# Kernel optimization log

Hardware: AMD Instinct MI355X
Metric: run time of the kernel (lower is better)

## Reference

```python
import jax, jax.numpy as jnp
import numpy as np
import math

D_MODEL = 1024
NUM_HEADS = 16
D_HEAD = D_MODEL // NUM_HEADS
SEQ = 2048
BATCH = 2
THETA = 10000.0
SCALE = 1.0 / math.sqrt(D_HEAD)


def rope_cos_sin(seq_len, d_head, theta):
    # freqs_cis equivalent: angles[t, j] = t * theta**(-2j/d_head)
    inv_freq = 1.0 / (theta ** (jnp.arange(0, d_head, 2, dtype=jnp.float32) / d_head))
    t = jnp.arange(seq_len, dtype=jnp.float32)
    ang = jnp.outer(t, inv_freq)  # [S, d_head//2]
    return jnp.cos(ang), jnp.sin(ang)


def apply_rope(x, cos, sin):
    # x: [B, S, H, Dh]; treat consecutive pairs as complex numbers
    B, S, H, Dh = x.shape
    xr = x.reshape(B, S, H, Dh // 2, 2)
    x0, x1 = xr[..., 0], xr[..., 1]
    c = cos[None, :, None, :]
    s = sin[None, :, None, :]
    out = jnp.stack([x0 * c - x1 * s, x0 * s + x1 * c], axis=-1)
    return out.reshape(B, S, H, Dh)


def setup_inputs() -> dict:
    key = jax.random.key(0)
    ks = jax.random.split(key, 9)
    w_std = 0.02
    return {
        "qkv": jax.random.normal(ks[0], (BATCH, SEQ, D_MODEL), jnp.float32),
        "Wq": jax.random.normal(ks[1], (D_MODEL, D_MODEL), jnp.float32) * w_std,
        "bq": jax.random.normal(ks[2], (D_MODEL,), jnp.float32) * w_std,
        "Wk": jax.random.normal(ks[3], (D_MODEL, D_MODEL), jnp.float32) * w_std,
        "bk": jax.random.normal(ks[4], (D_MODEL,), jnp.float32) * w_std,
        "Wv": jax.random.normal(ks[5], (D_MODEL, D_MODEL), jnp.float32) * w_std,
        "bv": jax.random.normal(ks[6], (D_MODEL,), jnp.float32) * w_std,
        "Wo": jax.random.normal(ks[7], (D_MODEL, D_MODEL), jnp.float32) * w_std,
        "bo": jax.random.normal(ks[8], (D_MODEL,), jnp.float32) * w_std,
    }


def reference(qkv, Wq, bq, Wk, bk, Wv, bv, Wo, bo):
    B, S, D = qkv.shape
    cos, sin = rope_cos_sin(S, D_HEAD, THETA)
    # torch Linear: y = x @ W.T + b
    q = (qkv @ Wq.T + bq).reshape(B, S, NUM_HEADS, D_HEAD)
    k = (qkv @ Wk.T + bk).reshape(B, S, NUM_HEADS, D_HEAD)
    v = (qkv @ Wv.T + bv).reshape(B, S, NUM_HEADS, D_HEAD)
    q = apply_rope(q, cos, sin)
    k = apply_rope(k, cos, sin)
    scores = jnp.einsum("bqhd,bkhd->bhqk", q, k) * SCALE
    causal = jnp.triu(jnp.ones((S, S), dtype=bool), k=1)
    scores = jnp.where(causal[None, None], -1e30, scores)
    attn = jax.nn.softmax(scores, axis=-1)
    out = jnp.einsum("bhqk,bkhd->bqhd", attn, v).reshape(B, S, D)
    return out @ Wo.T + bo
```

## Files before the change

### kernel.cpp

```cpp
#include <hip/hip_runtime.h>
#include <hip/hip_bf16.h>
#include <stdint.h>
#include <math.h>


typedef __bf16 bf16;
typedef __attribute__((ext_vector_type(4))) __bf16 bf16x4;
typedef __attribute__((ext_vector_type(8))) __bf16 bf16x8;
typedef __attribute__((ext_vector_type(4))) float f32x4;
typedef __attribute__((ext_vector_type(16))) float f32x16;
typedef __attribute__((ext_vector_type(4))) uint32_t u32x4;

#define SEQN 2048
#define DMOD 1024
#define NHEAD 16
#define DHEAD 64
#define MTOT 4096
#define VSTR 2080
#define QSCALE_LOG2E 0.18033688011112042f

__device__ __forceinline__ void gload_lds16(const bf16* g, bf16* l) {
  __builtin_amdgcn_global_load_lds(
      (const __attribute__((address_space(1))) uint32_t*)g,
      (__attribute__((address_space(3))) uint32_t*)l,
      16, 0, 0);
}

__device__ __forceinline__ uint32_t cvtpk(float lo, float hi) {
  uint32_t r;
  asm("v_cvt_pk_bf16_f32 %0, %1, %2" : "=v"(r) : "v"(lo), "v"(hi));
  return r;
}

__global__ __launch_bounds__(256) void prep_kernel(
    const float* __restrict__ X,
    const float* __restrict__ Wq, const float* __restrict__ Wk,
    const float* __restrict__ Wv, const float* __restrict__ Wo,
    bf16* __restrict__ Xb, bf16* __restrict__ Wqb, bf16* __restrict__ Wkb,
    bf16* __restrict__ Wvb, bf16* __restrict__ Wob,
    float* __restrict__ ctab, float* __restrict__ stab)
{
  const int tid = blockIdx.x * blockDim.x + threadIdx.x;
  const int nth = gridDim.x * blockDim.x;

  const float4* X4 = (const float4*)X;
  for (int i = tid; i < MTOT * DMOD / 4; i += nth) {
    float4 v = X4[i];
    bf16x4 o = { (bf16)v.x, (bf16)v.y, (bf16)v.z, (bf16)v.w };
    *(bf16x4*)(Xb + (size_t)i * 4) = o;
  }
  const float4* q4 = (const float4*)Wq;
  const float4* k4 = (const float4*)Wk;
  const float4* v4 = (const float4*)Wv;
  const float4* o4 = (const float4*)Wo;
  for (int i = tid; i < DMOD * DMOD / 4; i += nth) {
    float4 a = q4[i];
    float4 b = k4[i];
    float4 c = v4[i];
    float4 d = o4[i];
    *(bf16x4*)(Wqb + (size_t)i * 4) = bf16x4{ (bf16)a.x, (bf16)a.y, (bf16)a.z, (bf16)a.w };
    *(bf16x4*)(Wkb + (size_t)i * 4) = bf16x4{ (bf16)b.x, (bf16)b.y, (bf16)b.z, (bf16)b.w };
    *(bf16x4*)(Wvb + (size_t)i * 4) = bf16x4{ (bf16)c.x, (bf16)c.y, (bf16)c.z, (bf16)c.w };
    *(bf16x4*)(Wob + (size_t)i * 4) = bf16x4{ (bf16)d.x, (bf16)d.y, (bf16)d.z, (bf16)d.w };
  }
  for (int i = tid; i < SEQN * 32; i += nth) {
    const int s = i >> 5, p = i & 31;
    const float invf = (float)pow(10000.0, -(double)p / 32.0);
    const float ang = (float)s * invf;
    float sv, cv;
    sincosf(ang, &sv, &cv);
    ctab[i] = cv;
    stab[i] = sv;
  }
}

__global__ __launch_bounds__(256) void gemm_qkv(
    const bf16* __restrict__ Xb,
    const bf16* __restrict__ Wqb, const bf16* __restrict__ Wkb, const bf16* __restrict__ Wvb,
    const float* __restrict__ bq, const float* __restrict__ bk, const float* __restrict__ bv,
    const float* __restrict__ ctab, const float* __restrict__ stab,
    bf16* __restrict__ Qb, bf16* __restrict__ Kb, bf16* __restrict__ Vtb)
{
  __shared__ bf16 sA[128 * 32];
  __shared__ bf16 sB[128 * 32];

  const int z = blockIdx.z;
  const bf16* Bm = (z == 0) ? Wqb : (z == 1) ? Wkb : Wvb;
  const float* bias = (z == 0) ? bq : (z == 1) ? bk : bv;

  const int t = threadIdx.x;
  const int lane = t & 63, l15 = lane & 15, g = lane >> 4;
  const int wave = t >> 6, wm = wave >> 1, wn = wave & 1;
  const int tileM = blockIdx.y * 128, tileN = blockIdx.x * 128;

  f32x4 acc[4][4] = {};

  const int srow = t >> 2, schk = t & 3;
  const bf16* gA = Xb + (size_t)(tileM + srow) * DMOD + schk * 8;
  const bf16* gB = Bm + (size_t)(tileN + srow) * DMOD + schk * 8;
  bf16* lA = sA + t * 8;
  bf16* lB = sB + t * 8;

  for (int k0 = 0; k0 < DMOD; k0 += 32) {
    __syncthreads();
    gload_lds16(gA + k0, lA);
    gload_lds16(gA + k0 + 64 * DMOD, lA + 2048);
    gload_lds16(gB + k0, lB);
    gload_lds16(gB + k0 + 64 * DMOD, lB + 2048);
    __syncthreads();
    bf16x8 af[4], bfr[4];
#pragma unroll
    for (int i = 0; i < 4; ++i)
      af[i] = *(const bf16x8*)(sA + (wm * 64 + i * 16 + l15) * 32 + g * 8);
#pragma unroll
    for (int j = 0; j < 4; ++j)
      bfr[j] = *(const bf16x8*)(sB + (wn * 64 + j * 16 + l15) * 32 + g * 8);
#pragma unroll
    for (int i = 0; i < 4; ++i)
#pragma unroll
      for (int j = 0; j < 4; ++j)
        acc[i][j] = __builtin_amdgcn_mfma_f32_16x16x32_bf16(af[i], bfr[j], acc[i][j], 0, 0, 0);
  }

#pragma unroll
  for (int j = 0; j < 4; ++j) {
    const int col = tileN + wn * 64 + j * 16 + l15;
    const float bcol = bias[col];
    const int h = col >> 6, d = col & 63;
#pragma unroll
    for (int i = 0; i < 4; ++i) {
#pragma unroll
      for (int r = 0; r < 4; ++r) {
        const int row = tileM + wm * 64 + i * 16 + g * 4 + r;
        const int b = row >> 11, s = row & (SEQN - 1);
        const float v = acc[i][j][r] + bcol;
        if (z != 2) {
          const int pair = d >> 1;
          const float cv = ctab[s * 32 + pair];
          const float sv = stab[s * 32 + pair];
          const float partner = __shfl_xor(v, 1);
          float rv = (d & 1) ? (partner * sv + v * cv) : (v * cv - partner * sv);
          if (z == 0) rv *= QSCALE_LOG2E;
          bf16* dst = (z == 0) ? Qb : Kb;
          dst[(((size_t)(b * NHEAD + h)) * SEQN + s) * DHEAD + d] = (bf16)rv;
        } else {
          Vtb[(((size_t)(b * NHEAD + h)) * DHEAD + d) * VSTR + s] = (bf16)v;
        }
      }
    }
  }
}

__global__ __launch_bounds__(256, 1) void attn_kernel(
    const bf16* __restrict__ Qb, const bf16* __restrict__ Kb,
    const bf16* __restrict__ Vt, bf16* __restrict__ AO)
{
  const int t = threadIdx.x;
  const int lane = t & 63, l31 = lane & 31, hi = lane >> 5;
  const int wave = t >> 6;

  const int bid = blockIdx.x;
  const int p = bid >> 5, bh = bid & 31;

  const bf16* Kp = Kb + (size_t)bh * SEQN * DHEAD;
  const bf16* Vp = Vt + (size_t)bh * DHEAD * VSTR;
  const bf16* Qp = Qb + (size_t)bh * SEQN * DHEAD;
  const int b = bh >> 4, h = bh & 15;

  auto prefetch = [&](bf16x8 (&K)[2][4], bf16x8 (&V)[2][4], int kv0) {
#pragma unroll
    for (int s = 0; s < 2; ++s)
#pragma unroll
      for (int ch = 0; ch < 4; ++ch)
        K[s][ch] = *(const bf16x8*)(Kp + (size_t)(kv0 + 32 * s + l31) * DHEAD + 16 * ch + 8 * hi);
#pragma unroll
    for (int dblk = 0; dblk < 2; ++dblk)
#pragma unroll
      for (int c = 0; c < 4; ++c)
        V[dblk][c] = *(const bf16x8*)(Vp + (size_t)(dblk * 32 + l31) * VSTR + kv0 + 16 * c + 8 * hi);
  };

  auto run_phase = [&](int qtile, int wrow) {
    const int qbase = qtile * 128 + wrow * 32;
    const int qg = qbase + l31;
    const int niter = (qbase >> 6) + 1;

    bf16x8 qf[4];
#pragma unroll
    for (int ch = 0; ch < 4; ++ch)
      qf[ch] = *(const bf16x8*)(Qp + (size_t)qg * DHEAD + 16 * ch + 8 * hi);

    f32x16 a0 = {}, a1 = {};
    float m = -1e30f, l = 0.f;

    auto compute = [&](const bf16x8 (&K)[2][4], const bf16x8 (&V)[2][4], int kv0) {
      f32x16 s0 = {}, s1 = {};
#pragma unroll
      for (int ch = 0; ch < 4; ++ch) {
        s0 = __builtin_amdgcn_mfma_f32_32x32x16_bf16(K[0][ch], qf[ch], s0, 0, 0, 0);
        s1 = __builtin_amdgcn_mfma_f32_32x32x16_bf16(K[1][ch], qf[ch], s1, 0, 0, 0);
      }
      float tv[32];
#pragma unroll
      for (int i = 0; i < 16; ++i) { tv[i] = s0[i]; tv[16 + i] = s1[i]; }

      if (kv0 + 63 > qbase) {
#pragma unroll
        for (int i = 0; i < 32; ++i) {
          const int key = kv0 + 32 * (i >> 4) + ((i & 3) + 8 * ((i >> 2) & 3) + 4 * hi);
          if (key > qg) tv[i] = -1e30f;
        }
      }

      float red[16];
#pragma unroll
      for (int i = 0; i < 16; ++i) red[i] = fmaxf(tv[i], tv[i + 16]);
#pragma unroll
      for (int st = 8; st >= 1; st >>= 1)
#pragma unroll
        for (int i = 0; i < st; ++i) red[i] = fmaxf(red[i], red[i + st]);
      const float tmax = fmaxf(red[0], __shfl_xor(red[0], 32));
      const float mnew = fmaxf(m, tmax);
      const float alpha = __builtin_amdgcn_exp2f(m - mnew);
      m = mnew;

#pragma unroll
      for (int i = 0; i < 32; ++i) tv[i] = __builtin_amdgcn_exp2f(tv[i] - mnew);
#pragma unroll
      for (int i = 0; i < 16; ++i) red[i] = tv[i] + tv[i + 16];
#pragma unroll
      for (int st = 8; st >= 1; st >>= 1)
#pragma unroll
        for (int i = 0; i < st; ++i) red[i] += red[i + st];
      l = l * alpha + (red[0] + __shfl_xor(red[0], 32));

#pragma unroll
      for (int i = 0; i < 16; ++i) { a0[i] *= alpha; a1[i] *= alpha; }

#pragma unroll
      for (int c = 0; c < 4; ++c) {
        const int b0 = (c & 1) * 8 + (c >> 1) * 16;
        const uint32_t P0  = cvtpk(tv[b0 + 0], tv[b0 + 1]);
        const uint32_t P0b = cvtpk(tv[b0 + 2], tv[b0 + 3]);
        const uint32_t P1  = cvtpk(tv[b0 + 4], tv[b0 + 5]);
        const uint32_t P1b = cvtpk(tv[b0 + 6], tv[b0 + 7]);
        const uint32_t sP0  = (uint32_t)__shfl_xor((int)P0, 32);
        const uint32_t sP0b = (uint32_t)__shfl_xor((int)P0b, 32);
        const uint32_t sP1  = (uint32_t)__shfl_xor((int)P1, 32);
        const uint32_t sP1b = (uint32_t)__shfl_xor((int)P1b, 32);
        u32x4 pw;
        pw[0] = hi ? sP1  : P0;
        pw[1] = hi ? sP1b : P0b;
        pw[2] = hi ? P1   : sP0;
        pw[3] = hi ? P1b  : sP0b;
        const bf16x8 pf = __builtin_bit_cast(bf16x8, pw);
        a0 = __builtin_amdgcn_mfma_f32_32x32x16_bf16(V[0][c], pf, a0, 0, 0, 0);
        a1 = __builtin_amdgcn_mfma_f32_32x32x16_bf16(V[1][c], pf, a1, 0, 0, 0);
      }
    };

    bf16x8 kA[2][4], vA[2][4], kB[2][4], vB[2][4];
    prefetch(kA, vA, 0);
    int it = 0;
    for (; it + 1 < niter; it += 2) {
      prefetch(kB, vB, (it + 1) * 64);
      compute(kA, vA, it * 64);
      if (it + 2 < niter) prefetch(kA, vA, (it + 2) * 64);
      compute(kB, vB, (it + 1) * 64);
    }
    if (it < niter) compute(kA, vA, it * 64);

    const float linv = 1.f / l;
    const size_t rowoff = ((size_t)(b * SEQN + qg)) * DMOD + h * DHEAD;
#pragma unroll
    for (int dblk = 0; dblk < 2; ++dblk) {
      const f32x16& av = dblk ? a1 : a0;
#pragma unroll
      for (int rg = 0; rg < 4; ++rg) {
        const int d0 = dblk * 32 + rg * 8 + 4 * hi;
        bf16x4 ov = { (bf16)(av[rg * 4 + 0] * linv), (bf16)(av[rg * 4 + 1] * linv),
                      (bf16)(av[rg * 4 + 2] * linv), (bf16)(av[rg * 4 + 3] * linv) };
        *(bf16x4*)(AO + rowoff + d0) = ov;
      }
    }
  };

  run_phase(p, wave);
  run_phase(15 - p, 3 - wave);
}

__global__ __launch_bounds__(256) void gemm_out(
    const bf16* __restrict__ AO, const bf16* __restrict__ Wob,
    const float* __restrict__ bo, float* __restrict__ out)
{
  __shared__ bf16 sA[128 * 32];
  __shared__ bf16 sB[128 * 32];

  const int t = threadIdx.x;
  const int lane = t & 63, l15 = lane & 15, g = lane >> 4;
  const int wave = t >> 6, wm = wave >> 1, wn = wave & 1;
  const int tileM = blockIdx.y * 128, tileN = blockIdx.x * 128;

  f32x4 acc[4][4] = {};

  const int srow = t >> 2, schk = t & 3;
  const bf16* gA = AO + (size_t)(tileM + srow) * DMOD + schk * 8;
  const bf16* gB = Wob + (size_t)(tileN + srow) * DMOD + schk * 8;
  bf16* lA = sA + t * 8;
  bf16* lB = sB + t * 8;

  for (int k0 = 0; k0 < DMOD; k0 += 32) {
    __syncthreads();
    gload_lds16(gA + k0, lA);
    gload_lds16(gA + k0 + 64 * DMOD, lA + 2048);
    gload_lds16(gB + k0, lB);
    gload_lds16(gB + k0 + 64 * DMOD, lB + 2048);
    __syncthreads();
    bf16x8 af[4], bfr[4];
#pragma unroll
    for (int i = 0; i < 4; ++i)
      af[i] = *(const bf16x8*)(sA + (wm * 64 + i * 16 + l15) * 32 + g * 8);
#pragma unroll
    for (int j = 0; j < 4; ++j)
      bfr[j] = *(const bf16x8*)(sB + (wn * 64 + j * 16 + l15) * 32 + g * 8);
#pragma unroll
    for (int i = 0; i < 4; ++i)
#pragma unroll
      for (int j = 0; j < 4; ++j)
        acc[i][j] = __builtin_amdgcn_mfma_f32_16x16x32_bf16(af[i], bfr[j], acc[i][j], 0, 0, 0);
  }

#pragma unroll
  for (int j = 0; j < 4; ++j) {
    const int col = tileN + wn * 64 + j * 16 + l15;
    const float bcol = bo[col];
#pragma unroll
    for (int i = 0; i < 4; ++i)
#pragma unroll
      for (int r = 0; r < 4; ++r) {
        const int row = tileM + wm * 64 + i * 16 + g * 4 + r;
        out[(size_t)row * DMOD + col] = acc[i][j][r] + bcol;
      }
  }
}

extern "C" void kernel_launch(void* const* d_in, const int* in_sizes, int n_in,
                              void* d_out, int out_size, void* d_ws, size_t ws_size,
                              hipStream_t stream)
{
  (void)in_sizes; (void)n_in; (void)out_size; (void)ws_size;
  const float* X  = (const float*)d_in[0];
  const float* Wq = (const float*)d_in[1];
  const float* bq = (const float*)d_in[2];
  const float* Wk = (const float*)d_in[3];
  const float* bk = (const float*)d_in[4];
  const float* Wv = (const float*)d_in[5];
  const float* bv = (const float*)d_in[6];
  const float* Wo = (const float*)d_in[7];
  const float* bo = (const float*)d_in[8];

  char* ws = (char*)d_ws;
  float* ctab = (float*)(ws + 0);
  float* stab = (float*)(ws + 262144);
  bf16* Xb  = (bf16*)(ws + 524288);
  bf16* Wqb = (bf16*)(ws + 8912896);
  bf16* Wkb = (bf16*)(ws + 11010048);
  bf16* Wvb = (bf16*)(ws + 13107200);
  bf16* Wob = (bf16*)(ws + 15204352);
  bf16* Qb  = (bf16*)(ws + 17301504);
  bf16* Kb  = (bf16*)(ws + 25690112);
  bf16* Vtb = (bf16*)(ws + 34078720);
  bf16* AO  = (bf16*)(ws + 42598400);

  prep_kernel<<<1024, 256, 0, stream>>>(X, Wq, Wk, Wv, Wo, Xb, Wqb, Wkb, Wvb, Wob, ctab, stab);
  gemm_qkv<<<dim3(8, 32, 3), 256, 0, stream>>>(Xb, Wqb, Wkb, Wvb, bq, bk, bv, ctab, stab, Qb, Kb, Vtb);
  attn_kernel<<<256, 256, 0, stream>>>(Qb, Kb, Vtb, AO);
  gemm_out<<<dim3(8, 32), 256, 0, stream>>>(AO, Wob, bo, (float*)d_out);
}
```

Baseline: 162.9 us.

## Triple-buffer LDS tiles in QKV and output GEMMs with async prefetch

Both projection GEMMs now use three LDS stages and issue global-to-LDS loads two K-steps ahead. Explicit vmcnt waits and raw barriers replace the load-then-sync pattern, so memory latency overlaps with MFMA work instead of stalling every K iteration. This triples shared memory use per block (48 KB), which may lower occupancy, and it depends on the vmcnt accounting being correct.

```diff
diff --git a/kernel.cpp b/kernel.cpp
--- a/kernel.cpp
+++ b/kernel.cpp
@@ -81,8 +81,8 @@
     const float* __restrict__ ctab, const float* __restrict__ stab,
     bf16* __restrict__ Qb, bf16* __restrict__ Kb, bf16* __restrict__ Vtb)
 {
-  __shared__ bf16 sA[128 * 32];
-  __shared__ bf16 sB[128 * 32];
+  __shared__ bf16 sA[3][128 * 32];
+  __shared__ bf16 sB[3][128 * 32];
 
   const int z = blockIdx.z;
   const bf16* Bm = (z == 0) ? Wqb : (z == 1) ? Wkb : Wvb;
@@ -95,31 +95,52 @@
 
   f32x4 acc[4][4] = {};
 
-  const int srow = t >> 2, schk = t & 3;
-  const bf16* gA = Xb + (size_t)(tileM + srow) * DMOD + schk * 8;
-  const bf16* gB = Bm + (size_t)(tileN + srow) * DMOD + schk * 8;
-  bf16* lA = sA + t * 8;
-  bf16* lB = sB + t * 8;
-
-  for (int k0 = 0; k0 < DMOD; k0 += 32) {
-    __syncthreads();
-    gload_lds16(gA + k0, lA);
-    gload_lds16(gA + k0 + 64 * DMOD, lA + 2048);
-    gload_lds16(gB + k0, lB);
-    gload_lds16(gB + k0 + 64 * DMOD, lB + 2048);
-    __syncthreads();
+  const bf16* gA = Xb + (size_t)(tileM + (t >> 2)) * DMOD + (t & 3) * 8;
+  const bf16* gB = Bm + (size_t)(tileN + (t >> 2)) * DMOD + (t & 3) * 8;
+
+  auto stage = [&](int buf, int k0) {
+    gload_lds16(gA + k0, &sA[buf][t * 8]);
+    gload_lds16(gA + k0 + 64 * DMOD, &sA[buf][2048 + t * 8]);
+    gload_lds16(gB + k0, &sB[buf][t * 8]);
+    gload_lds16(gB + k0 + 64 * DMOD, &sB[buf][2048 + t * 8]);
+  };
+
+  stage(0, 0);
+  stage(1, 32);
+
+  const int NS = DMOD / 32;
+  int cur = 0;
+  for (int s = 0; s < NS; ++s) {
+    if (s + 2 < NS) {
+      int pf = cur + 2; if (pf >= 3) pf -= 3;
+      stage(pf, (s + 2) * 32);
+      asm volatile("s_waitcnt vmcnt(8)" ::: "memory");
+    } else if (s + 1 < NS) {
+      asm volatile("s_waitcnt vmcnt(4)" ::: "memory");
+    } else {
+      asm volatile("s_waitcnt vmcnt(0)" ::: "memory");
+    }
+    __builtin_amdgcn_s_barrier();
+    asm volatile("" ::: "memory");
+
+    const bf16* cA = sA[cur];
+    const bf16* cB = sB[cur];
     bf16x8 af[4], bfr[4];
 #pragma unroll
     for (int i = 0; i < 4; ++i)
-      af[i] = *(const bf16x8*)(sA + (wm * 64 + i * 16 + l15) * 32 + g * 8);
+      af[i] = *(const bf16x8*)(cA + (wm * 64 + i * 16 + l15) * 32 + g * 8);
 #pragma unroll
     for (int j = 0; j < 4; ++j)
-      bfr[j] = *(const bf16x8*)(sB + (wn * 64 + j * 16 + l15) * 32 + g * 8);
+      bfr[j] = *(const bf16x8*)(cB + (wn * 64 + j * 16 + l15) * 32 + g * 8);
 #pragma unroll
     for (int i = 0; i < 4; ++i)
 #pragma unroll
       for (int j = 0; j < 4; ++j)
         acc[i][j] = __builtin_amdgcn_mfma_f32_16x16x32_bf16(af[i], bfr[j], acc[i][j], 0, 0, 0);
+
+    asm volatile("" ::: "memory");
+    __builtin_amdgcn_s_barrier();
+    cur = (cur == 2) ? 0 : cur + 1;
   }
 
 #pragma unroll
@@ -293,8 +314,8 @@
     const bf16* __restrict__ AO, const bf16* __restrict__ Wob,
     const float* __restrict__ bo, float* __restrict__ out)
 {
-  __shared__ bf16 sA[128 * 32];
-  __shared__ bf16 sB[128 * 32];
+  __shared__ bf16 sA[3][128 * 32];
+  __shared__ bf16 sB[3][128 * 32];
 
   const int t = threadIdx.x;
   const int lane = t & 63, l15 = lane & 15, g = lane >> 4;
@@ -303,31 +324,52 @@
 
   f32x4 acc[4][4] = {};
 
-  const int srow = t >> 2, schk = t & 3;
-  const bf16* gA = AO + (size_t)(tileM + srow) * DMOD + schk * 8;
-  const bf16* gB = Wob + (size_t)(tileN + srow) * DMOD + schk * 8;
-  bf16* lA = sA + t * 8;
-  bf16* lB = sB + t * 8;
-
-  for (int k0 = 0; k0 < DMOD; k0 += 32) {
-    __syncthreads();
-    gload_lds16(gA + k0, lA);
-    gload_lds16(gA + k0 + 64 * DMOD, lA + 2048);
-    gload_lds16(gB + k0, lB);
-    gload_lds16(gB + k0 + 64 * DMOD, lB + 2048);
-    __syncthreads();
+  const bf16* gA = AO + (size_t)(tileM + (t >> 2)) * DMOD + (t & 3) * 8;
+  const bf16* gB = Wob + (size_t)(tileN + (t >> 2)) * DMOD + (t & 3) * 8;
+
+  auto stage = [&](int buf, int k0) {
+    gload_lds16(gA + k0, &sA[buf][t * 8]);
+    gload_lds16(gA + k0 + 64 * DMOD, &sA[buf][2048 + t * 8]);
+    gload_lds16(gB + k0, &sB[buf][t * 8]);
+    gload_lds16(gB + k0 + 64 * DMOD, &sB[buf][2048 + t * 8]);
+  };
+
+  stage(0, 0);
+  stage(1, 32);
+
+  const int NS = DMOD / 32;
+  int cur = 0;
+  for (int s = 0; s < NS; ++s) {
+    if (s + 2 < NS) {
+      int pf = cur + 2; if (pf >= 3) pf -= 3;
+      stage(pf, (s + 2) * 32);
+      asm volatile("s_waitcnt vmcnt(8)" ::: "memory");
+    } else if (s + 1 < NS) {
+      asm volatile("s_waitcnt vmcnt(4)" ::: "memory");
+    } else {
+      asm volatile("s_waitcnt vmcnt(0)" ::: "memory");
+    }
+    __builtin_amdgcn_s_barrier();
+    asm volatile("" ::: "memory");
+
+    const bf16* cA = sA[cur];
+    const bf16* cB = sB[cur];
     bf16x8 af[4], bfr[4];
 #pragma unroll
     for (int i = 0; i < 4; ++i)
-      af[i] = *(const bf16x8*)(sA + (wm * 64 + i * 16 + l15) * 32 + g * 8);
+      af[i] = *(const bf16x8*)(cA + (wm * 64 + i * 16 + l15) * 32 + g * 8);
 #pragma unroll
     for (int j = 0; j < 4; ++j)
-      bfr[j] = *(const bf16x8*)(sB + (wn * 64 + j * 16 + l15) * 32 + g * 8);
+      bfr[j] = *(const bf16x8*)(cB + (wn * 64 + j * 16 + l15) * 32 + g * 8);
 #pragma unroll
     for (int i = 0; i < 4; ++i)
 #pragma unroll
       for (int j = 0; j < 4; ++j)
         acc[i][j] = __builtin_amdgcn_mfma_f32_16x16x32_bf16(af[i], bfr[j], acc[i][j], 0, 0, 0);
+
+    asm volatile("" ::: "memory");
+    __builtin_amdgcn_s_barrier();
+    cur = (cur == 2) ? 0 : cur + 1;
   }
 
 #pragma unroll
```

Result: faster. 142.0 us (-12.8%).
